# Performance work log

Measured on AMD Instinct MI355X. Metric: run time of the kernel, lower is better.

Reference implementation:

```python
import jax, jax.numpy as jnp
import numpy as np

RES = 300
NC = 48
N_PTS = 1_000_000


def _bilinear2d(params, gx, gy):
    """params: (C,R,R); gx,gy: (N,) in [-1,1]. grid_sample align_corners=True,
    gx indexes width (last axis), gy indexes height."""
    C, R, _ = params.shape
    px = (gx + 1.0) * 0.5 * (R - 1)
    py = (gy + 1.0) * 0.5 * (R - 1)
    x0f = jnp.floor(px)
    y0f = jnp.floor(py)
    wx = px - x0f
    wy = py - y0f
    x0 = jnp.clip(x0f.astype(jnp.int32), 0, R - 1)
    x1 = jnp.clip(x0 + 1, 0, R - 1)
    y0 = jnp.clip(y0f.astype(jnp.int32), 0, R - 1)
    y1 = jnp.clip(y0 + 1, 0, R - 1)
    f00 = params[:, y0, x0]  # (C,N)
    f01 = params[:, y0, x1]
    f10 = params[:, y1, x0]
    f11 = params[:, y1, x1]
    return (f00 * (1 - wx) * (1 - wy) + f01 * wx * (1 - wy)
            + f10 * (1 - wx) * wy + f11 * wx * wy)


def _linear1d(params, gy):
    """params: (C,R) (line grid with width 1, x-coord fixed at 0); gy: (N,)."""
    C, R = params.shape
    py = (gy + 1.0) * 0.5 * (R - 1)
    y0f = jnp.floor(py)
    wy = py - y0f
    y0 = jnp.clip(y0f.astype(jnp.int32), 0, R - 1)
    y1 = jnp.clip(y0 + 1, 0, R - 1)
    return params[:, y0] * (1 - wy) + params[:, y1] * wy  # (C,N)


def setup_inputs() -> dict:
    key = jax.random.key(0)
    k1, k2, k3 = jax.random.split(key, 3)
    x = jax.random.uniform(k1, (N_PTS, 3), dtype=jnp.float32)
    plane_params = 0.1 * jax.random.normal(k2, (3, NC, RES, RES), dtype=jnp.float32)
    line_params = 0.1 * jax.random.normal(k3, (3, NC, RES, 1), dtype=jnp.float32)
    return {"x": x, "plane_params": plane_params, "line_params": line_params}


def reference(x, plane_params, line_params):
    N = x.shape[0]
    xs = 2.0 * x - 1.0  # (N,3)
    # grid_sample grid is (x_coord, y_coord): plane pairs [0,1],[0,2],[1,2]
    gx = jnp.stack([xs[:, 0], xs[:, 0], xs[:, 1]])  # (3,N) width coord
    gy = jnp.stack([xs[:, 1], xs[:, 2], xs[:, 2]])  # (3,N) height coord
    gl = jnp.stack([xs[:, 2], xs[:, 1], xs[:, 0]])  # (3,N) line coord
    plane_f = jax.vmap(_bilinear2d)(plane_params, gx, gy)      # (3,C,N)
    line_f = jax.vmap(_linear1d)(line_params[..., 0], gl)      # (3,C,N)
    feats = (plane_f * line_f).reshape(3 * NC, N).T            # (N, 3C)
    return feats
```

## Files before the change

### kernel.cpp

```cpp
#include <hip/hip_runtime.h>
#include <hip/hip_fp16.h>

#define RES 300
#define NC 48
#define RES2 (RES * RES)

typedef float f32x4 __attribute__((ext_vector_type(4)));
typedef unsigned int u32x4 __attribute__((ext_vector_type(4)));

struct alignas(8) h4 { __half2 a, b; };

__device__ __forceinline__ int clampi(int v, int lo, int hi) {
    return v < lo ? lo : (v > hi ? hi : v);
}

__global__ __launch_bounds__(256) void tp_planes_kernel(const float* __restrict__ in,
                                                        __half* __restrict__ out) {
    unsigned idx = blockIdx.x * 256u + threadIdx.x;
    if (idx >= 3u * RES2) return;
    unsigned p  = idx / RES2;
    unsigned yx = idx - p * RES2;
    const float* src = in + (size_t)p * NC * RES2 + yx;
    unsigned short v[NC];
#pragma unroll
    for (int c = 0; c < NC; ++c) {
        __half h = __float2half(src[(size_t)c * RES2]);
        v[c] = *reinterpret_cast<unsigned short*>(&h);
    }
    u32x4* dst = reinterpret_cast<u32x4*>(out + (size_t)idx * NC);
#pragma unroll
    for (int i = 0; i < 6; ++i) {
        u32x4 w;
        w.x = (unsigned)v[8 * i + 0] | ((unsigned)v[8 * i + 1] << 16);
        w.y = (unsigned)v[8 * i + 2] | ((unsigned)v[8 * i + 3] << 16);
        w.z = (unsigned)v[8 * i + 4] | ((unsigned)v[8 * i + 5] << 16);
        w.w = (unsigned)v[8 * i + 6] | ((unsigned)v[8 * i + 7] << 16);
        dst[i] = w;
    }
}

__global__ __launch_bounds__(256) void tp_lines_kernel(const float* __restrict__ in,
                                                       __half* __restrict__ out) {
    unsigned idx = blockIdx.x * 256u + threadIdx.x;
    if (idx >= 3u * RES) return;
    unsigned p = idx / RES;
    unsigned y = idx - p * RES;
#pragma unroll
    for (int c = 0; c < NC; ++c)
        out[(size_t)idx * NC + c] = __float2half(in[((size_t)p * NC + c) * RES + y]);
}

__global__ __launch_bounds__(256) void encode_kernel(const float* __restrict__ x,
                                                     const __half* __restrict__ pt,
                                                     const __half* __restrict__ lt,
                                                     float* __restrict__ out,
                                                     unsigned N) {
    unsigned gid = blockIdx.x * 256u + threadIdx.x;
    if (gid >= N * 36u) return;
    unsigned n  = gid / 36u;
    unsigned q  = gid - n * 36u;
    unsigned p  = q / 12u;
    unsigned c4 = q - p * 12u;

    float xv0 = x[3u * n + 0u];
    float xv1 = x[3u * n + 1u];
    float xv2 = x[3u * n + 2u];

    float gxv = (p == 2u) ? xv1 : xv0;
    float gyv = (p == 0u) ? xv1 : xv2;
    float glv = (p == 0u) ? xv2 : ((p == 1u) ? xv1 : xv0);

    float gxs = 2.0f * gxv - 1.0f;
    float gys = 2.0f * gyv - 1.0f;
    float gls = 2.0f * glv - 1.0f;
    float px = (gxs + 1.0f) * 0.5f * (float)(RES - 1);
    float py = (gys + 1.0f) * 0.5f * (float)(RES - 1);
    float pl = (gls + 1.0f) * 0.5f * (float)(RES - 1);

    float x0f = floorf(px), y0f = floorf(py), l0f = floorf(pl);
    float wx = px - x0f, wy = py - y0f, wl = pl - l0f;

    int ix0 = clampi((int)x0f, 0, RES - 1);
    int ix1 = ix0 + 1 > RES - 1 ? RES - 1 : ix0 + 1;
    int iy0 = clampi((int)y0f, 0, RES - 1);
    int iy1 = iy0 + 1 > RES - 1 ? RES - 1 : iy0 + 1;
    int il0 = clampi((int)l0f, 0, RES - 1);
    int il1 = il0 + 1 > RES - 1 ? RES - 1 : il0 + 1;

    unsigned cbase = c4 * 4u;
    const __half* pb = pt + (size_t)p * RES2 * NC;
    unsigned o00 = ((unsigned)iy0 * RES + (unsigned)ix0) * NC + cbase;
    unsigned o01 = ((unsigned)iy0 * RES + (unsigned)ix1) * NC + cbase;
    unsigned o10 = ((unsigned)iy1 * RES + (unsigned)ix0) * NC + cbase;
    unsigned o11 = ((unsigned)iy1 * RES + (unsigned)ix1) * NC + cbase;

    h4 v00 = *reinterpret_cast<const h4*>(pb + o00);
    h4 v01 = *reinterpret_cast<const h4*>(pb + o01);
    h4 v10 = *reinterpret_cast<const h4*>(pb + o10);
    h4 v11 = *reinterpret_cast<const h4*>(pb + o11);

    float2 f00a = __half22float2(v00.a), f00b = __half22float2(v00.b);
    float2 f01a = __half22float2(v01.a), f01b = __half22float2(v01.b);
    float2 f10a = __half22float2(v10.a), f10b = __half22float2(v10.b);
    float2 f11a = __half22float2(v11.a), f11b = __half22float2(v11.b);

    float w00 = (1.0f - wx) * (1.0f - wy);
    float w01 = wx * (1.0f - wy);
    float w10 = (1.0f - wx) * wy;
    float w11 = wx * wy;

    f32x4 plane_v;
    plane_v.x = f00a.x * w00 + f01a.x * w01 + f10a.x * w10 + f11a.x * w11;
    plane_v.y = f00a.y * w00 + f01a.y * w01 + f10a.y * w10 + f11a.y * w11;
    plane_v.z = f00b.x * w00 + f01b.x * w01 + f10b.x * w10 + f11b.x * w11;
    plane_v.w = f00b.y * w00 + f01b.y * w01 + f10b.y * w10 + f11b.y * w11;

    const __half* lb = lt + (size_t)p * RES * NC + cbase;
    h4 vl0 = *reinterpret_cast<const h4*>(lb + (size_t)il0 * NC);
    h4 vl1 = *reinterpret_cast<const h4*>(lb + (size_t)il1 * NC);
    float2 l0a = __half22float2(vl0.a), l0b = __half22float2(vl0.b);
    float2 l1a = __half22float2(vl1.a), l1b = __half22float2(vl1.b);

    float wl0 = 1.0f - wl;
    f32x4 line_v;
    line_v.x = l0a.x * wl0 + l1a.x * wl;
    line_v.y = l0a.y * wl0 + l1a.y * wl;
    line_v.z = l0b.x * wl0 + l1b.x * wl;
    line_v.w = l0b.y * wl0 + l1b.y * wl;

    f32x4 r = plane_v * line_v;

    __builtin_nontemporal_store(r, reinterpret_cast<f32x4*>(out + (size_t)n * 144u + (size_t)q * 4u));
}

__global__ __launch_bounds__(256) void encode_fallback_kernel(const float* __restrict__ x,
                                                              const float* __restrict__ plane,
                                                              const float* __restrict__ line,
                                                              float* __restrict__ out,
                                                              unsigned N) {
    unsigned gid = blockIdx.x * 256u + threadIdx.x;
    if (gid >= N * 36u) return;
    unsigned n  = gid / 36u;
    unsigned q  = gid - n * 36u;
    unsigned p  = q / 12u;
    unsigned c4 = q - p * 12u;

    float xv0 = x[3u * n + 0u];
    float xv1 = x[3u * n + 1u];
    float xv2 = x[3u * n + 2u];
    float gxv = (p == 2u) ? xv1 : xv0;
    float gyv = (p == 0u) ? xv1 : xv2;
    float glv = (p == 0u) ? xv2 : ((p == 1u) ? xv1 : xv0);

    float gxs = 2.0f * gxv - 1.0f;
    float gys = 2.0f * gyv - 1.0f;
    float gls = 2.0f * glv - 1.0f;
    float px = (gxs + 1.0f) * 0.5f * (float)(RES - 1);
    float py = (gys + 1.0f) * 0.5f * (float)(RES - 1);
    float pl = (gls + 1.0f) * 0.5f * (float)(RES - 1);

    float x0f = floorf(px), y0f = floorf(py), l0f = floorf(pl);
    float wx = px - x0f, wy = py - y0f, wl = pl - l0f;

    int ix0 = clampi((int)x0f, 0, RES - 1);
    int ix1 = ix0 + 1 > RES - 1 ? RES - 1 : ix0 + 1;
    int iy0 = clampi((int)y0f, 0, RES - 1);
    int iy1 = iy0 + 1 > RES - 1 ? RES - 1 : iy0 + 1;
    int il0 = clampi((int)l0f, 0, RES - 1);
    int il1 = il0 + 1 > RES - 1 ? RES - 1 : il0 + 1;

    float w00 = (1.0f - wx) * (1.0f - wy);
    float w01 = wx * (1.0f - wy);
    float w10 = (1.0f - wx) * wy;
    float w11 = wx * wy;
    float wl0 = 1.0f - wl;

    float4 r;
    float* rp = &r.x;
#pragma unroll
    for (int cc = 0; cc < 4; ++cc) {
        unsigned c = c4 * 4u + (unsigned)cc;
        const float* pp = plane + ((size_t)p * NC + c) * RES2;
        float f00 = pp[(size_t)iy0 * RES + ix0];
        float f01 = pp[(size_t)iy0 * RES + ix1];
        float f10 = pp[(size_t)iy1 * RES + ix0];
        float f11 = pp[(size_t)iy1 * RES + ix1];
        float pv = f00 * w00 + f01 * w01 + f10 * w10 + f11 * w11;
        const float* lp = line + ((size_t)p * NC + c) * RES;
        float lv = lp[il0] * wl0 + lp[il1] * wl;
        rp[cc] = pv * lv;
    }
    *reinterpret_cast<float4*>(out + (size_t)n * 144u + (size_t)q * 4u) = r;
}

extern "C" void kernel_launch(void* const* d_in, const int* in_sizes, int n_in,
                              void* d_out, int out_size, void* d_ws, size_t ws_size,
                              hipStream_t stream) {
    const float* x     = (const float*)d_in[0];
    const float* plane = (const float*)d_in[1];
    const float* line  = (const float*)d_in[2];
    float* out = (float*)d_out;
    unsigned N = (unsigned)(in_sizes[0] / 3);

    size_t plane_t_elems = (size_t)3 * RES2 * NC;
    size_t line_t_elems  = (size_t)3 * RES * NC;
    size_t need = (plane_t_elems + line_t_elems) * sizeof(__half);

    unsigned total  = N * 36u;
    unsigned blocks = (total + 255u) / 256u;

    if (ws_size >= need) {
        __half* plane_t = (__half*)d_ws;
        __half* line_t  = plane_t + plane_t_elems;
        tp_planes_kernel<<<(3u * RES2 + 255u) / 256u, 256, 0, stream>>>(plane, plane_t);
        tp_lines_kernel<<<(3u * RES + 255u) / 256u, 256, 0, stream>>>(line, line_t);
        encode_kernel<<<blocks, 256, 0, stream>>>(x, plane_t, line_t, out, N);
    } else {
        encode_fallback_kernel<<<blocks, 256, 0, stream>>>(x, plane, line, out, N);
    }
}
```

Baseline: 313.9 us.

## Sort points by Morton key before encoding to improve gather locality

Result: faster. 293.5 us (-6.5%).

```diff
diff --git a/kernel.cpp b/kernel.cpp
--- a/kernel.cpp
+++ b/kernel.cpp
@@ -4,6 +4,7 @@
 #define RES 300
 #define NC 48
 #define RES2 (RES * RES)
+#define NBINS 32768
 
 typedef float f32x4 __attribute__((ext_vector_type(4)));
 typedef unsigned int u32x4 __attribute__((ext_vector_type(4)));
@@ -13,6 +14,22 @@
 __device__ __forceinline__ int clampi(int v, int lo, int hi) {
     return v < lo ? lo : (v > hi ? hi : v);
 }
+
+__device__ __forceinline__ unsigned spread5(unsigned v) {
+    v &= 31u;
+    v = (v | (v << 8)) & 0x100Fu;
+    v = (v | (v << 4)) & 0x10C3u;
+    v = (v | (v << 2)) & 0x1249u;
+    return v;
+}
+
+__device__ __forceinline__ unsigned morton_key(float a, float b, float c) {
+    int ca = clampi((int)(a * 32.0f), 0, 31);
+    int cb = clampi((int)(b * 32.0f), 0, 31);
+    int cc = clampi((int)(c * 32.0f), 0, 31);
+    return spread5((unsigned)ca) | (spread5((unsigned)cb) << 1) | (spread5((unsigned)cc) << 2);
+}
+
 
 __global__ __launch_bounds__(256) void tp_planes_kernel(const float* __restrict__ in,
                                                         __half* __restrict__ out) {
@@ -49,6 +66,153 @@
     for (int c = 0; c < NC; ++c)
         out[(size_t)idx * NC + c] = __float2half(in[((size_t)p * NC + c) * RES + y]);
 }
+
+
+__global__ __launch_bounds__(256) void zero_bins_kernel(unsigned* __restrict__ counts) {
+    unsigned i = blockIdx.x * 256u + threadIdx.x;
+    if (i < NBINS) counts[i] = 0u;
+}
+
+__global__ __launch_bounds__(256) void hist_kernel(const float* __restrict__ x,
+                                                   unsigned* __restrict__ counts,
+                                                   unsigned N) {
+    unsigned i = blockIdx.x * 256u + threadIdx.x;
+    if (i >= N) return;
+    unsigned k = morton_key(x[3u * i], x[3u * i + 1u], x[3u * i + 2u]);
+    atomicAdd(&counts[k], 1u);
+}
+
+__global__ __launch_bounds__(1024) void scan_kernel(const unsigned* __restrict__ counts,
+                                                    unsigned* __restrict__ offs) {
+    __shared__ unsigned part[1024];
+    int t = threadIdx.x;
+    unsigned local[NBINS / 1024];
+    unsigned s = 0;
+#pragma unroll
+    for (int j = 0; j < NBINS / 1024; ++j) {
+        local[j] = counts[t * (NBINS / 1024) + j];
+        s += local[j];
+    }
+    part[t] = s;
+    __syncthreads();
+    for (int d = 1; d < 1024; d <<= 1) {
+        unsigned v = (t >= d) ? part[t - d] : 0u;
+        __syncthreads();
+        part[t] += v;
+        __syncthreads();
+    }
+    unsigned run = (t == 0) ? 0u : part[t - 1];
+#pragma unroll
+    for (int j = 0; j < NBINS / 1024; ++j) {
+        offs[t * (NBINS / 1024) + j] = run;
+        run += local[j];
+    }
+}
+
+__global__ __launch_bounds__(256) void scatter_kernel(const float* __restrict__ x,
+                                                      unsigned* __restrict__ offs,
+                                                      f32x4* __restrict__ sorted,
+                                                      unsigned N) {
+    unsigned i = blockIdx.x * 256u + threadIdx.x;
+    if (i >= N) return;
+    float a = x[3u * i], b = x[3u * i + 1u], c = x[3u * i + 2u];
+    unsigned k = morton_key(a, b, c);
+    unsigned pos = atomicAdd(&offs[k], 1u);
+    f32x4 v;
+    v.x = a; v.y = b; v.z = c; v.w = __uint_as_float(i);
+    sorted[pos] = v;
+}
+
+
+__global__ __launch_bounds__(256) void encode_sorted_kernel(const f32x4* __restrict__ sorted,
+                                                            const __half* __restrict__ pt,
+                                                            const __half* __restrict__ lt,
+                                                            float* __restrict__ out,
+                                                            unsigned N) {
+    unsigned nwg  = gridDim.x;
+    unsigned orig = blockIdx.x;
+    unsigned xcd = orig & 7u, j = orig >> 3u;
+    unsigned qq = nwg >> 3u, r = nwg & 7u;
+    unsigned bid = (xcd < r ? xcd * (qq + 1u) : r * (qq + 1u) + (xcd - r) * qq) + j;
+
+    unsigned gid = bid * 256u + threadIdx.x;
+    if (gid >= N * 36u) return;
+    unsigned s  = gid / 36u;
+    unsigned q  = gid - s * 36u;
+    unsigned p  = q / 12u;
+    unsigned c4 = q - p * 12u;
+
+    f32x4 pv4 = sorted[s];
+    float xv0 = pv4.x, xv1 = pv4.y, xv2 = pv4.z;
+    unsigned n = __float_as_uint(pv4.w);
+
+    float gxv = (p == 2u) ? xv1 : xv0;
+    float gyv = (p == 0u) ? xv1 : xv2;
+    float glv = (p == 0u) ? xv2 : ((p == 1u) ? xv1 : xv0);
+
+    float gxs = 2.0f * gxv - 1.0f;
+    float gys = 2.0f * gyv - 1.0f;
+    float gls = 2.0f * glv - 1.0f;
+    float px = (gxs + 1.0f) * 0.5f * (float)(RES - 1);
+    float py = (gys + 1.0f) * 0.5f * (float)(RES - 1);
+    float pl = (gls + 1.0f) * 0.5f * (float)(RES - 1);
+
+    float x0f = floorf(px), y0f = floorf(py), l0f = floorf(pl);
+    float wx = px - x0f, wy = py - y0f, wl = pl - l0f;
+
+    int ix0 = clampi((int)x0f, 0, RES - 1);
+    int ix1 = ix0 + 1 > RES - 1 ? RES - 1 : ix0 + 1;
+    int iy0 = clampi((int)y0f, 0, RES - 1);
+    int iy1 = iy0 + 1 > RES - 1 ? RES - 1 : iy0 + 1;
+    int il0 = clampi((int)l0f, 0, RES - 1);
+    int il1 = il0 + 1 > RES - 1 ? RES - 1 : il0 + 1;
+
+    unsigned cbase = c4 * 4u;
+    const __half* pb = pt + (size_t)p * RES2 * NC;
+    unsigned o00 = ((unsigned)iy0 * RES + (unsigned)ix0) * NC + cbase;
+    unsigned o01 = ((unsigned)iy0 * RES + (unsigned)ix1) * NC + cbase;
+    unsigned o10 = ((unsigned)iy1 * RES + (unsigned)ix0) * NC + cbase;
+    unsigned o11 = ((unsigned)iy1 * RES + (unsigned)ix1) * NC + cbase;
+
+    h4 v00 = *reinterpret_cast<const h4*>(pb + o00);
+    h4 v01 = *reinterpret_cast<const h4*>(pb + o01);
+    h4 v10 = *reinterpret_cast<const h4*>(pb + o10);
+    h4 v11 = *reinterpret_cast<const h4*>(pb + o11);
+
+    float2 f00a = __half22float2(v00.a), f00b = __half22float2(v00.b);
+    float2 f01a = __half22float2(v01.a), f01b = __half22float2(v01.b);
+    float2 f10a = __half22float2(v10.a), f10b = __half22float2(v10.b);
+    float2 f11a = __half22float2(v11.a), f11b = __half22float2(v11.b);
+
+    float w00 = (1.0f - wx) * (1.0f - wy);
+    float w01 = wx * (1.0f - wy);
+    float w10 = (1.0f - wx) * wy;
+    float w11 = wx * wy;
+
+    f32x4 plane_v;
+    plane_v.x = f00a.x * w00 + f01a.x * w01 + f10a.x * w10 + f11a.x * w11;
+    plane_v.y = f00a.y * w00 + f01a.y * w01 + f10a.y * w10 + f11a.y * w11;
+    plane_v.z = f00b.x * w00 + f01b.x * w01 + f10b.x * w10 + f11b.x * w11;
+    plane_v.w = f00b.y * w00 + f01b.y * w01 + f10b.y * w10 + f11b.y * w11;
+
+    const __half* lb = lt + (size_t)p * RES * NC + cbase;
+    h4 vl0 = *reinterpret_cast<const h4*>(lb + (size_t)il0 * NC);
+    h4 vl1 = *reinterpret_cast<const h4*>(lb + (size_t)il1 * NC);
+    float2 l0a = __half22float2(vl0.a), l0b = __half22float2(vl0.b);
+    float2 l1a = __half22float2(vl1.a), l1b = __half22float2(vl1.b);
+
+    float wl0 = 1.0f - wl;
+    f32x4 line_v;
+    line_v.x = l0a.x * wl0 + l1a.x * wl;
+    line_v.y = l0a.y * wl0 + l1a.y * wl;
+    line_v.z = l0b.x * wl0 + l1b.x * wl;
+    line_v.w = l0b.y * wl0 + l1b.y * wl;
+
+    f32x4 rr = plane_v * line_v;
+
+    __builtin_nontemporal_store(rr, reinterpret_cast<f32x4*>(out + (size_t)n * 144u + (size_t)q * 4u));
+}
+
 
 __global__ __launch_bounds__(256) void encode_kernel(const float* __restrict__ x,
                                                      const __half* __restrict__ pt,
@@ -65,7 +229,6 @@
     float xv0 = x[3u * n + 0u];
     float xv1 = x[3u * n + 1u];
     float xv2 = x[3u * n + 2u];
-
     float gxv = (p == 2u) ? xv1 : xv0;
     float gyv = (p == 0u) ? xv1 : xv2;
     float glv = (p == 0u) ? xv2 : ((p == 1u) ? xv1 : xv0);
@@ -89,15 +252,10 @@
 
     unsigned cbase = c4 * 4u;
     const __half* pb = pt + (size_t)p * RES2 * NC;
-    unsigned o00 = ((unsigned)iy0 * RES + (unsigned)ix0) * NC + cbase;
-    unsigned o01 = ((unsigned)iy0 * RES + (unsigned)ix1) * NC + cbase;
-    unsigned o10 = ((unsigned)iy1 * RES + (unsigned)ix0) * NC + cbase;
-    unsigned o11 = ((unsigned)iy1 * RES + (unsigned)ix1) * NC + cbase;
-
-    h4 v00 = *reinterpret_cast<const h4*>(pb + o00);
-    h4 v01 = *reinterpret_cast<const h4*>(pb + o01);
-    h4 v10 = *reinterpret_cast<const h4*>(pb + o10);
-    h4 v11 = *reinterpret_cast<const h4*>(pb + o11);
+    h4 v00 = *reinterpret_cast<const h4*>(pb + ((unsigned)iy0 * RES + (unsigned)ix0) * NC + cbase);
+    h4 v01 = *reinterpret_cast<const h4*>(pb + ((unsigned)iy0 * RES + (unsigned)ix1) * NC + cbase);
+    h4 v10 = *reinterpret_cast<const h4*>(pb + ((unsigned)iy1 * RES + (unsigned)ix0) * NC + cbase);
+    h4 v11 = *reinterpret_cast<const h4*>(pb + ((unsigned)iy1 * RES + (unsigned)ix1) * NC + cbase);
 
     float2 f00a = __half22float2(v00.a), f00b = __half22float2(v00.b);
     float2 f01a = __half22float2(v01.a), f01b = __half22float2(v01.b);
@@ -128,9 +286,8 @@
     line_v.z = l0b.x * wl0 + l1b.x * wl;
     line_v.w = l0b.y * wl0 + l1b.y * wl;
 
-    f32x4 r = plane_v * line_v;
-
-    __builtin_nontemporal_store(r, reinterpret_cast<f32x4*>(out + (size_t)n * 144u + (size_t)q * 4u));
+    f32x4 rr = plane_v * line_v;
+    __builtin_nontemporal_store(rr, reinterpret_cast<f32x4*>(out + (size_t)n * 144u + (size_t)q * 4u));
 }
 
 __global__ __launch_bounds__(256) void encode_fallback_kernel(const float* __restrict__ x,
@@ -204,12 +361,34 @@
 
     size_t plane_t_elems = (size_t)3 * RES2 * NC;
     size_t line_t_elems  = (size_t)3 * RES * NC;
-    size_t need = (plane_t_elems + line_t_elems) * sizeof(__half);
+    size_t sorted_bytes  = (size_t)N * 16u;
+    size_t plane_bytes   = plane_t_elems * sizeof(__half);
+    size_t line_bytes    = line_t_elems * sizeof(__half);
+    size_t bins_bytes    = (size_t)NBINS * 4u;
+
+    size_t need_mid  = plane_bytes + line_bytes;
+    size_t need_full = sorted_bytes + plane_bytes + line_bytes + 2u * bins_bytes;
 
     unsigned total  = N * 36u;
     unsigned blocks = (total + 255u) / 256u;
-
-    if (ws_size >= need) {
+    unsigned pblocks = (N + 255u) / 256u;
+
+    if (ws_size >= need_full) {
+        char* base = (char*)d_ws;
+        f32x4*   sorted  = (f32x4*)base;                      base += sorted_bytes;
+        __half*  plane_t = (__half*)base;                     base += plane_bytes;
+        __half*  line_t  = (__half*)base;                     base += line_bytes;
+        unsigned* counts = (unsigned*)base;                   base += bins_bytes;
+        unsigned* offs   = (unsigned*)base;
+
+        zero_bins_kernel<<<(NBINS + 255) / 256, 256, 0, stream>>>(counts);
+        hist_kernel<<<pblocks, 256, 0, stream>>>(x, counts, N);
+        tp_planes_kernel<<<(3u * RES2 + 255u) / 256u, 256, 0, stream>>>(plane, plane_t);
+        tp_lines_kernel<<<(3u * RES + 255u) / 256u, 256, 0, stream>>>(line, line_t);
+        scan_kernel<<<1, 1024, 0, stream>>>(counts, offs);
+        scatter_kernel<<<pblocks, 256, 0, stream>>>(x, offs, sorted, N);
+        encode_sorted_kernel<<<blocks, 256, 0, stream>>>(sorted, plane_t, line_t, out, N);
+    } else if (ws_size >= need_mid) {
         __half* plane_t = (__half*)d_ws;
         __half* line_t  = plane_t + plane_t_elems;
         tp_planes_kernel<<<(3u * RES2 + 255u) / 256u, 256, 0, stream>>>(plane, plane_t);
```
